# Kernel optimization log

Measured on AMD Instinct MI355X. Metric: run time of the kernel, lower is better.

Reference implementation:

```python
import jax, jax.numpy as jnp
import numpy as np

B = 128          # batch (requests)
SPEC = 4         # drafts per request (uniform here, code handles ragged)
V = 128000       # vocab size
MAX_SPEC_LEN = SPEC
NT = B * SPEC    # total flattened draft tokens
PLACEHOLDER = -1


def setup_inputs() -> dict:
    key = jax.random.key(0)
    k1, k2, k3, k4, k5 = jax.random.split(key, 5)
    draft_token_ids = jax.random.randint(k1, (NT,), 0, V, dtype=jnp.int32)
    draft_probs = jax.nn.softmax(2.0 * jax.random.normal(k2, (NT, V), dtype=jnp.float32), axis=-1)
    target_probs = jax.nn.softmax(2.0 * jax.random.normal(k3, (NT, V), dtype=jnp.float32), axis=-1)
    uniform_probs = jax.random.uniform(k4, (NT,), dtype=jnp.float32)
    bonus_token_ids = jax.random.randint(k5, (B,), 0, V, dtype=jnp.int32)
    cu_num_draft_tokens = (jnp.arange(1, B + 1) * SPEC).astype(jnp.int32)
    return {
        "draft_probs": draft_probs,
        "target_probs": target_probs,
        "uniform_probs": uniform_probs,
        "draft_token_ids": draft_token_ids,
        "cu_num_draft_tokens": cu_num_draft_tokens,
        "bonus_token_ids": bonus_token_ids,
    }


def reference(draft_probs, target_probs, uniform_probs, draft_token_ids,
              cu_num_draft_tokens, bonus_token_ids):
    # Faithful vectorized version of rejection_random_sample_kernel.
    nt = target_probs.shape[0]
    L = MAX_SPEC_LEN
    cu = cu_num_draft_tokens.astype(jnp.int32)
    prev = jnp.concatenate([jnp.zeros((1,), cu.dtype), cu[:-1]])   # start_idx per req
    ndraft = cu - prev                                              # [B]
    pos = jnp.arange(L, dtype=jnp.int32)                            # [L]
    tok_idx = prev[:, None] + pos[None, :]                          # [B,L] global token idx
    valid = pos[None, :] < ndraft[:, None]                          # [B,L]
    safe_idx = jnp.clip(tok_idx, 0, nt - 1)

    d_ids = draft_token_ids[safe_idx]                               # [B,L]
    tp = target_probs[safe_idx, d_ids]                              # target prob of draft token
    dp = draft_probs[safe_idx, d_ids]                               # draft prob of draft token
    uu = uniform_probs[safe_idx]

    # neutral values outside valid range: ratio=1, uniform=1 keep carries unchanged
    ratio = jnp.where(valid & (dp > 0), tp / jnp.where(dp > 0, dp, 1.0), 1.0)
    uu = jnp.where(valid, uu, 1.0)
    dpos = valid & (dp > 0)

    def step(carry, xs):
        pi, U = carry                       # [B] each
        r, u, ok = xs
        pi = jnp.minimum(pi * r, 1.0)
        U = U * u
        accept = ok & (pi >= U)
        return (pi, U), accept

    init = (jnp.ones((cu.shape[0],), jnp.float32), jnp.ones((cu.shape[0],), jnp.float32))
    _, accept = jax.lax.scan(step, init, (ratio.T, uu.T, dpos.T))   # accept: [L,B]
    accept = accept.T                                                # [B,L]

    # last accepted position (or -1); 'rejected' == final-iteration accept failed
    last = jnp.max(jnp.where(accept, pos[None, :], -1), axis=1)      # [B]
    rejected = (ndraft > 0) & (last != ndraft - 1)

    # copy accepted draft tokens [0..last]
    out_L = jnp.where(pos[None, :] <= last[:, None], d_ids, PLACEHOLDER).astype(jnp.int32)
    out = jnp.concatenate([out_L, jnp.full((cu.shape[0], 1), PLACEHOLDER, jnp.int32)], axis=1)

    # recovered token: argmax of target_probs row at position last+1
    rec_row = jnp.clip(prev + last + 1, 0, nt - 1)
    rec_id = jnp.argmax(target_probs[rec_row], axis=-1).astype(jnp.int32)   # [B]

    write_col = jnp.where(rejected, last + 1, ndraft)
    write_val = jnp.where(rejected, rec_id, bonus_token_ids.astype(jnp.int32))
    out = out.at[jnp.arange(cu.shape[0]), write_col].set(write_val)
    return out
```

## Files before the change

### kernel.cpp

```cpp
#include <hip/hip_runtime.h>
#include <hip/hip_bf16.h>
#include <float.h>

#define SPLITS 16


__global__ void chain_kernel(
    const float* __restrict__ draft_probs,
    const float* __restrict__ target_probs,
    const float* __restrict__ uniform_probs,
    const int*   __restrict__ draft_ids,
    const int*   __restrict__ cu,
    const int*   __restrict__ bonus,
    int*         __restrict__ out,
    unsigned long long* __restrict__ packed,
    int* __restrict__ flag, int* __restrict__ recrow, int* __restrict__ writecol,
    int B, int V, int NT, int L)
{
    const int b = blockIdx.x * blockDim.x + threadIdx.x;
    if (b >= B) return;

    const int start = (b == 0) ? 0 : cu[b - 1];
    const int nd    = cu[b] - start;
    const int nchain = (nd < L) ? nd : L;

    float pi = 1.0f, U = 1.0f;
    int last = -1;
    int* row = out + (size_t)b * (L + 1);

    for (int i = 0; i < nchain; ++i) {
        const int t   = start + i;
        const int did = draft_ids[t];
        row[i] = did;
        const size_t off = (size_t)t * (size_t)V + (size_t)did;
        const float tp = target_probs[off];
        const float dp = draft_probs[off];
        const float uu = uniform_probs[t];
        const bool ok = dp > 0.0f;
        const float r = ok ? (tp / dp) : 1.0f;
        pi = fminf(pi * r, 1.0f);
        U  = U * uu;
        if (ok && pi >= U) last = i;
    }
    for (int i = last + 1; i <= L; ++i) row[i] = -1;

    const bool rejected = (nd > 0) && (last != nd - 1);
    if (!rejected) {
        row[nd] = bonus[b];
    }
    int rr = start + last + 1;
    rr = rr < 0 ? 0 : (rr > NT - 1 ? NT - 1 : rr);

    flag[b]     = rejected ? 1 : 0;
    recrow[b]   = rr;
    writecol[b] = last + 1;
    packed[b]   = 0ull;
}

__global__ __launch_bounds__(256) void argmax_partial_kernel(
    const float* __restrict__ target_probs,
    const unsigned long long* __restrict__ ,
    unsigned long long* __restrict__ packed,
    const int* __restrict__ flag, const int* __restrict__ recrow,
    int V)
{
    const int b = blockIdx.x;
    const int s = blockIdx.y;
    if (!flag[b]) return;

    const int tid = threadIdx.x;
    const float* rowbase = target_probs + (size_t)recrow[b] * (size_t)V;
    const int n4 = V >> 2;
    const int chunk4 = (n4 + SPLITS - 1) / SPLITS;
    const int lo4 = s * chunk4;
    const int hi4 = (lo4 + chunk4 < n4) ? lo4 + chunk4 : n4;

    float bestv = -FLT_MAX;
    int   besti = 0x7fffffff;
    const float4* rowp = (const float4*)rowbase;
    for (int j = lo4 + tid; j < hi4; j += 256) {
        const float4 v = rowp[j];
        const int base = j << 2;
        if (v.x > bestv) { bestv = v.x; besti = base;     }
        if (v.y > bestv) { bestv = v.y; besti = base + 1; }
        if (v.z > bestv) { bestv = v.z; besti = base + 2; }
        if (v.w > bestv) { bestv = v.w; besti = base + 3; }
    }
    if (s == SPLITS - 1) {
        for (int j = (n4 << 2) + tid; j < V; j += 256) {
            const float v = rowbase[j];
            if (v > bestv) { bestv = v; besti = j; }
        }
    }

    __shared__ float sv[256];
    __shared__ int   si[256];
    sv[tid] = bestv;
    si[tid] = besti;
    __syncthreads();
    for (int w = 128; w > 0; w >>= 1) {
        if (tid < w) {
            const float ov = sv[tid + w];
            const int   oi = si[tid + w];
            if (ov > sv[tid] || (ov == sv[tid] && oi < si[tid])) {
                sv[tid] = ov;
                si[tid] = oi;
            }
        }
        __syncthreads();
    }
    if (tid == 0 && sv[0] > -FLT_MAX) {
        const unsigned int fbits = __float_as_uint(sv[0]);
        const unsigned long long p =
            ((unsigned long long)fbits << 32) |
            (unsigned long long)(0xFFFFFFFFu - (unsigned int)si[0]);
        atomicMax(&packed[b], p);
    }
}

__global__ void finalize_kernel(
    int* __restrict__ out,
    const unsigned long long* __restrict__ packed,
    const int* __restrict__ flag, const int* __restrict__ writecol,
    int B, int L)
{
    const int b = blockIdx.x * blockDim.x + threadIdx.x;
    if (b >= B) return;
    if (!flag[b]) return;
    const unsigned long long p = packed[b];
    const int idx = (int)(0xFFFFFFFFu - (unsigned int)(p & 0xFFFFFFFFull));
    out[(size_t)b * (L + 1) + writecol[b]] = idx;
}

extern "C" void kernel_launch(void* const* d_in, const int* in_sizes, int n_in,
                              void* d_out, int out_size, void* d_ws, size_t ws_size,
                              hipStream_t stream) {
    const float* draft_probs   = (const float*)d_in[0];
    const float* target_probs  = (const float*)d_in[1];
    const float* uniform_probs = (const float*)d_in[2];
    const int*   draft_ids     = (const int*)d_in[3];
    const int*   cu            = (const int*)d_in[4];
    const int*   bonus         = (const int*)d_in[5];
    int*         out           = (int*)d_out;

    const int NT = in_sizes[2];
    const int V  = in_sizes[0] / NT;
    const int B  = in_sizes[4];
    const int L  = out_size / B - 1;

    unsigned long long* packed = (unsigned long long*)d_ws;
    int* flag     = (int*)((char*)d_ws + (size_t)B * 8);
    int* recrow   = (int*)((char*)d_ws + (size_t)B * 8 + (size_t)B * 4);
    int* writecol = (int*)((char*)d_ws + (size_t)B * 8 + (size_t)B * 8);

    const int bthreads = 256;
    const int bblocks  = (B + bthreads - 1) / bthreads;

    chain_kernel<<<bblocks, bthreads, 0, stream>>>(
        draft_probs, target_probs, uniform_probs, draft_ids, cu, bonus,
        out, packed, flag, recrow, writecol, B, V, NT, L);

    dim3 grid(B, SPLITS);
    argmax_partial_kernel<<<grid, 256, 0, stream>>>(
        target_probs, nullptr, packed, flag, recrow, V);

    finalize_kernel<<<bblocks, bthreads, 0, stream>>>(
        out, packed, flag, writecol, B, L);
}
```

Before: 408.4 us.

## Fuse finalize into argmax via last-block counter and batch chain loads

```diff
diff --git a/kernel.cpp b/kernel.cpp
--- a/kernel.cpp
+++ b/kernel.cpp
@@ -3,6 +3,7 @@
 #include <float.h>
 
 #define SPLITS 16
+#define MAXP   8
 
 
 __global__ void chain_kernel(
@@ -14,6 +15,7 @@
     const int*   __restrict__ bonus,
     int*         __restrict__ out,
     unsigned long long* __restrict__ packed,
+    unsigned int* __restrict__ count,
     int* __restrict__ flag, int* __restrict__ recrow, int* __restrict__ writecol,
     int B, int V, int NT, int L)
 {
@@ -24,30 +26,62 @@
     const int nd    = cu[b] - start;
     const int nchain = (nd < L) ? nd : L;
 
+    int   did[MAXP];
+    float uu[MAXP], tp[MAXP], dp[MAXP];
+    const int np = (nchain < MAXP) ? nchain : MAXP;
+
+    #pragma unroll
+    for (int i = 0; i < MAXP; ++i) {
+        if (i < np) {
+            did[i] = draft_ids[start + i];
+            uu[i]  = uniform_probs[start + i];
+        }
+    }
+    #pragma unroll
+    for (int i = 0; i < MAXP; ++i) {
+        if (i < np) {
+            const size_t off = (size_t)(start + i) * (size_t)V + (size_t)did[i];
+            tp[i] = target_probs[off];
+            dp[i] = draft_probs[off];
+        }
+    }
+
     float pi = 1.0f, U = 1.0f;
     int last = -1;
     int* row = out + (size_t)b * (L + 1);
 
-    for (int i = 0; i < nchain; ++i) {
+    #pragma unroll
+    for (int i = 0; i < MAXP; ++i) {
+        if (i < np) {
+            const bool ok = dp[i] > 0.0f;
+            const float r = ok ? (tp[i] / dp[i]) : 1.0f;
+            pi = fminf(pi * r, 1.0f);
+            U  = U * uu[i];
+            if (ok && pi >= U) last = i;
+        }
+    }
+    for (int i = MAXP; i < nchain; ++i) {
         const int t   = start + i;
-        const int did = draft_ids[t];
-        row[i] = did;
-        const size_t off = (size_t)t * (size_t)V + (size_t)did;
-        const float tp = target_probs[off];
-        const float dp = draft_probs[off];
-        const float uu = uniform_probs[t];
-        const bool ok = dp > 0.0f;
-        const float r = ok ? (tp / dp) : 1.0f;
+        const int d   = draft_ids[t];
+        const size_t off = (size_t)t * (size_t)V + (size_t)d;
+        const float tpv = target_probs[off];
+        const float dpv = draft_probs[off];
+        const bool ok = dpv > 0.0f;
+        const float r = ok ? (tpv / dpv) : 1.0f;
         pi = fminf(pi * r, 1.0f);
-        U  = U * uu;
+        U  = U * uniform_probs[t];
         if (ok && pi >= U) last = i;
     }
-    for (int i = last + 1; i <= L; ++i) row[i] = -1;
+
+    for (int i = 0; i <= L; ++i) {
+        int v = -1;
+        if (i <= last) v = (i < MAXP) ? did[i] : draft_ids[start + i];
+        row[i] = v;
+    }
 
     const bool rejected = (nd > 0) && (last != nd - 1);
-    if (!rejected) {
-        row[nd] = bonus[b];
-    }
+    if (!rejected) row[nd] = bonus[b];
+
     int rr = start + last + 1;
     rr = rr < 0 ? 0 : (rr > NT - 1 ? NT - 1 : rr);
 
@@ -55,14 +89,17 @@
     recrow[b]   = rr;
     writecol[b] = last + 1;
     packed[b]   = 0ull;
+    count[b]    = 0u;
 }
 
-__global__ __launch_bounds__(256) void argmax_partial_kernel(
+__global__ __launch_bounds__(256) void argmax_kernel(
     const float* __restrict__ target_probs,
-    const unsigned long long* __restrict__ ,
+    int* __restrict__ out,
     unsigned long long* __restrict__ packed,
+    unsigned int* __restrict__ count,
     const int* __restrict__ flag, const int* __restrict__ recrow,
-    int V)
+    const int* __restrict__ writecol,
+    int V, int L)
 {
     const int b = blockIdx.x;
     const int s = blockIdx.y;
@@ -93,43 +130,37 @@
         }
     }
 
-    __shared__ float sv[256];
-    __shared__ int   si[256];
-    sv[tid] = bestv;
-    si[tid] = besti;
+    #pragma unroll
+    for (int off = 32; off > 0; off >>= 1) {
+        const float ov = __shfl_down(bestv, off, 64);
+        const int   oi = __shfl_down(besti, off, 64);
+        if (ov > bestv || (ov == bestv && oi < besti)) { bestv = ov; besti = oi; }
+    }
+    __shared__ float swv[4];
+    __shared__ int   swi[4];
+    const int wave = tid >> 6;
+    if ((tid & 63) == 0) { swv[wave] = bestv; swi[wave] = besti; }
     __syncthreads();
-    for (int w = 128; w > 0; w >>= 1) {
-        if (tid < w) {
-            const float ov = sv[tid + w];
-            const int   oi = si[tid + w];
-            if (ov > sv[tid] || (ov == sv[tid] && oi < si[tid])) {
-                sv[tid] = ov;
-                si[tid] = oi;
-            }
+
+    if (tid == 0) {
+        #pragma unroll
+        for (int w = 1; w < 4; ++w) {
+            const float ov = swv[w];
+            const int   oi = swi[w];
+            if (ov > bestv || (ov == bestv && oi < besti)) { bestv = ov; besti = oi; }
         }
-        __syncthreads();
+        const unsigned long long p =
+            ((unsigned long long)__float_as_uint(bestv) << 32) |
+            (unsigned long long)(0xFFFFFFFFu - (unsigned int)besti);
+        atomicMax(&packed[b], p);
+        __threadfence();
+        const unsigned int old = atomicAdd(&count[b], 1u);
+        if (old == SPLITS - 1) {
+            const unsigned long long fin = atomicAdd(&packed[b], 0ull);
+            const int idx = (int)(0xFFFFFFFFu - (unsigned int)(fin & 0xFFFFFFFFull));
+            out[(size_t)b * (L + 1) + writecol[b]] = idx;
+        }
     }
-    if (tid == 0 && sv[0] > -FLT_MAX) {
-        const unsigned int fbits = __float_as_uint(sv[0]);
-        const unsigned long long p =
-            ((unsigned long long)fbits << 32) |
-            (unsigned long long)(0xFFFFFFFFu - (unsigned int)si[0]);
-        atomicMax(&packed[b], p);
-    }
-}
-
-__global__ void finalize_kernel(
-    int* __restrict__ out,
-    const unsigned long long* __restrict__ packed,
-    const int* __restrict__ flag, const int* __restrict__ writecol,
-    int B, int L)
-{
-    const int b = blockIdx.x * blockDim.x + threadIdx.x;
-    if (b >= B) return;
-    if (!flag[b]) return;
-    const unsigned long long p = packed[b];
-    const int idx = (int)(0xFFFFFFFFu - (unsigned int)(p & 0xFFFFFFFFull));
-    out[(size_t)b * (L + 1) + writecol[b]] = idx;
 }
 
 extern "C" void kernel_launch(void* const* d_in, const int* in_sizes, int n_in,
@@ -148,22 +179,21 @@
     const int B  = in_sizes[4];
     const int L  = out_size / B - 1;
 
-    unsigned long long* packed = (unsigned long long*)d_ws;
-    int* flag     = (int*)((char*)d_ws + (size_t)B * 8);
-    int* recrow   = (int*)((char*)d_ws + (size_t)B * 8 + (size_t)B * 4);
-    int* writecol = (int*)((char*)d_ws + (size_t)B * 8 + (size_t)B * 8);
+    char* ws = (char*)d_ws;
+    unsigned long long* packed = (unsigned long long*)ws;          ws += (size_t)B * 8;
+    unsigned int*       count  = (unsigned int*)ws;                ws += (size_t)B * 4;
+    int*                flag   = (int*)ws;                          ws += (size_t)B * 4;
+    int*                recrow = (int*)ws;                          ws += (size_t)B * 4;
+    int*                writecol = (int*)ws;
 
     const int bthreads = 256;
     const int bblocks  = (B + bthreads - 1) / bthreads;
 
     chain_kernel<<<bblocks, bthreads, 0, stream>>>(
         draft_probs, target_probs, uniform_probs, draft_ids, cu, bonus,
-        out, packed, flag, recrow, writecol, B, V, NT, L);
+        out, packed, count, flag, recrow, writecol, B, V, NT, L);
 
     dim3 grid(B, SPLITS);
-    argmax_partial_kernel<<<grid, 256, 0, stream>>>(
-        target_probs, nullptr, packed, flag, recrow, V);
-
-    finalize_kernel<<<bblocks, bthreads, 0, stream>>>(
-        out, packed, flag, writecol, B, L);
+    argmax_kernel<<<grid, 256, 0, stream>>>(
+        target_probs, out, packed, count, flag, recrow, writecol, V, L);
 }
```

Result: slower. 425.3 us (+4.1%).
